# Kernel tuning notes

Hardware: AMD Instinct MI355X
Metric: run time of the kernel (lower is better)

Reference implementation:

```python
import jax, jax.numpy as jnp
import numpy as np

N = 100000
E = 1600000
IN, HID, OUT = 2, 32, 1

def setup_inputs() -> dict:
    key = jax.random.key(0)
    ks = jax.random.split(key, 12)
    x = jax.random.normal(ks[0], (N, IN), dtype=jnp.float32)
    edge_index = jax.random.randint(ks[1], (2, E), 0, N, dtype=jnp.int64)
    def lin(k, i, o):
        s = 1.0 / np.sqrt(i)
        return jax.random.uniform(k, (i, o), jnp.float32, -s, s)
    return {
        "x": x,
        "edge_index": edge_index,
        "w1": lin(ks[2], IN, HID), "b1": jnp.zeros((HID,), jnp.float32),
        "g1": jnp.ones((HID,), jnp.float32), "be1": jnp.zeros((HID,), jnp.float32),
        "w2": lin(ks[3], HID, HID), "b2": jnp.zeros((HID,), jnp.float32),
        "g2": jnp.ones((HID,), jnp.float32), "be2": jnp.zeros((HID,), jnp.float32),
        "w3": lin(ks[4], HID, OUT), "b3": jnp.zeros((OUT,), jnp.float32),
    }

def _gcn_conv(x, src, dst, norm, W, b):
    # x: [N, Fin] -> [N, Fout]; symmetric-normalized aggregation incl. self-loops
    h = x @ W                                  # [N, Fout]
    msg = h[src] * norm[:, None]               # gather + scale, [E+N, Fout]
    out = jax.ops.segment_sum(msg, dst, num_segments=N)  # scatter-add
    return out + b

def _layer_norm(x, g, b, eps=1e-5):
    mu = jnp.mean(x, axis=-1, keepdims=True)
    var = jnp.mean(jnp.square(x - mu), axis=-1, keepdims=True)
    return (x - mu) * jax.lax.rsqrt(var + eps) * g + b

def reference(x, edge_index, w1, b1, g1, be1, w2, b2, g2, be2, w3, b3):
    loops = jnp.arange(N, dtype=edge_index.dtype)
    src = jnp.concatenate([edge_index[0], loops])  # [E+N]
    dst = jnp.concatenate([edge_index[1], loops])
    deg = jax.ops.segment_sum(jnp.ones_like(src, dtype=x.dtype), dst, num_segments=N)
    dinv = jnp.where(deg > 0, jax.lax.rsqrt(deg), 0.0)
    norm = dinv[src] * dinv[dst]                   # [E+N]

    h = _gcn_conv(x, src, dst, norm, w1, b1)
    h = jax.nn.relu(_layer_norm(h, g1, be1))       # dropout = identity (eval)
    h = _gcn_conv(h, src, dst, norm, w2, b2)
    h = jax.nn.relu(_layer_norm(h, g2, be2))
    return _gcn_conv(h, src, dst, norm, w3, b3)
```

## Files before the change

kernel.cpp:

```cpp
#include <hip/hip_runtime.h>
#include <hip/hip_fp16.h>

constexpr int NN  = 100000;
constexpr int NE  = 1600000;
constexpr int NE4 = NE / 4;
constexpr int HID = 32;
constexpr int NPB = 128;
constexpr int NBIN = (NN + NPB - 1) / NPB;
constexpr int NB  = (NN + 255) / 256;

constexpr int NPART = 8;
constexpr int PPB   = (NBIN + NPART - 1) / NPART;
constexpr int NCHUNK = 120;
constexpr int CAP   = 16;
constexpr int QS    = CAP + 1;


__global__ __launch_bounds__(256) void k_binhist(const int* __restrict__ ei,
                                                 int* __restrict__ bincnt) {
  __shared__ int lh[NBIN];
  int t = threadIdx.x;
  for (int b = t; b < NBIN; b += 256) lh[b] = 0;
  __syncthreads();
  const int4* d4 = (const int4*)(ei + NE);
  for (int q = blockIdx.x * 256 + t; q < NE4; q += gridDim.x * 256) {
    int4 v = d4[q];
    atomicAdd(&lh[v.x >> 7], 1);
    atomicAdd(&lh[v.y >> 7], 1);
    atomicAdd(&lh[v.z >> 7], 1);
    atomicAdd(&lh[v.w >> 7], 1);
  }
  __syncthreads();
  for (int b = t; b < NBIN; b += 256) {
    int v = lh[b];
    if (v) atomicAdd(&bincnt[b], v);
  }
}

__global__ __launch_bounds__(1024) void k_binscan(const int* __restrict__ bincnt,
                                                  int* __restrict__ binptr,
                                                  int* __restrict__ cursor) {
  __shared__ int s[1024];
  int t = threadIdx.x;
  int v = (t < NBIN) ? bincnt[t] : 0;
  s[t] = v;
  __syncthreads();
#pragma unroll
  for (int off = 1; off < 1024; off <<= 1) {
    int add = (t >= off) ? s[t - off] : 0;
    __syncthreads();
    s[t] += add;
    __syncthreads();
  }
  if (t < NBIN) {
    int ex = s[t] - v;
    binptr[t] = ex;
    cursor[t] = ex;
  }
  if (t == NBIN - 1) binptr[NBIN] = s[t];
}

__global__ __launch_bounds__(256) void k_wcscatter(const int* __restrict__ ei,
                                                   int* __restrict__ cursor,
                                                   int* __restrict__ be) {
  __shared__ int q[PPB * QS];
  __shared__ int qn[PPB];
  int t = threadIdx.x;
  int part  = blockIdx.x & (NPART - 1);
  int chunk = blockIdx.x >> 3;
  int b0  = part * PPB;
  int bHi = min(b0 + PPB, NBIN);
  int nb  = bHi - b0;
  for (int b = t; b < nb; b += 256) qn[b] = 0;
  int q0 = (int)((long long)NE4 * chunk / NCHUNK);
  int q1 = (int)((long long)NE4 * (chunk + 1) / NCHUNK);
  const int4* d4 = (const int4*)(ei + NE);
  const int4* s4 = (const int4*)ei;
  __syncthreads();
  for (int qbase = q0; qbase < q1; qbase += 256) {
    int qi = qbase + t;
    int4 dv = make_int4(-1, -1, -1, -1);
    int4 sv = make_int4(0, 0, 0, 0);
    if (qi < q1) { dv = d4[qi]; sv = s4[qi]; }
    int val0 = 0, val1 = 0, val2 = 0, val3 = 0;
    int lb0 = 0, lb1 = 0, lb2 = 0, lb3 = 0;
    unsigned pend = 0;
    {
      int bkt = dv.x >> 7;
      if (dv.x >= 0 && bkt >= b0 && bkt < bHi) {
        val0 = sv.x | ((dv.x & (NPB - 1)) << 17);
        lb0 = bkt - b0;
        int slot = atomicAdd(&qn[lb0], 1);
        if (slot < CAP) q[lb0 * QS + slot] = val0; else pend |= 1u;
      }
    }
    {
      int bkt = dv.y >> 7;
      if (dv.y >= 0 && bkt >= b0 && bkt < bHi) {
        val1 = sv.y | ((dv.y & (NPB - 1)) << 17);
        lb1 = bkt - b0;
        int slot = atomicAdd(&qn[lb1], 1);
        if (slot < CAP) q[lb1 * QS + slot] = val1; else pend |= 2u;
      }
    }
    {
      int bkt = dv.z >> 7;
      if (dv.z >= 0 && bkt >= b0 && bkt < bHi) {
        val2 = sv.z | ((dv.z & (NPB - 1)) << 17);
        lb2 = bkt - b0;
        int slot = atomicAdd(&qn[lb2], 1);
        if (slot < CAP) q[lb2 * QS + slot] = val2; else pend |= 4u;
      }
    }
    {
      int bkt = dv.w >> 7;
      if (dv.w >= 0 && bkt >= b0 && bkt < bHi) {
        val3 = sv.w | ((dv.w & (NPB - 1)) << 17);
        lb3 = bkt - b0;
        int slot = atomicAdd(&qn[lb3], 1);
        if (slot < CAP) q[lb3 * QS + slot] = val3; else pend |= 8u;
      }
    }
    for (;;) {
      __syncthreads();
      for (int b = t; b < nb; b += 256) {
        int n = qn[b];
        if (n >= CAP) {
          int pos = atomicAdd(&cursor[b0 + b], CAP);
#pragma unroll
          for (int j = 0; j < CAP; j++) be[pos + j] = q[b * QS + j];
          qn[b] = 0;
        }
      }
      if (!__syncthreads_or(pend ? 1 : 0)) break;
      if (pend & 1u) {
        int slot = atomicAdd(&qn[lb0], 1);
        if (slot < CAP) { q[lb0 * QS + slot] = val0; pend &= ~1u; }
      }
      if (pend & 2u) {
        int slot = atomicAdd(&qn[lb1], 1);
        if (slot < CAP) { q[lb1 * QS + slot] = val1; pend &= ~2u; }
      }
      if (pend & 4u) {
        int slot = atomicAdd(&qn[lb2], 1);
        if (slot < CAP) { q[lb2 * QS + slot] = val2; pend &= ~4u; }
      }
      if (pend & 8u) {
        int slot = atomicAdd(&qn[lb3], 1);
        if (slot < CAP) { q[lb3 * QS + slot] = val3; pend &= ~8u; }
      }
    }
  }
  for (int b = t; b < nb; b += 256) {
    int n = qn[b];
    if (n > 0) {
      int pos = atomicAdd(&cursor[b0 + b], n);
      for (int j = 0; j < n; j++) be[pos + j] = q[b * QS + j];
    }
  }
}

__global__ __launch_bounds__(256) void k_sort(const int* __restrict__ binptr,
                                              const int* __restrict__ be,
                                              const float* __restrict__ x,
                                              int* __restrict__ csr,
                                              int* __restrict__ rowptr,
                                              int* __restrict__ deg,
                                              float* __restrict__ dinv,
                                              float* __restrict__ xs) {
  __shared__ int hist[NPB];
  __shared__ int excl[NPB];
  __shared__ int cur[NPB];
  int t = threadIdx.x, b = blockIdx.x;
  int e0 = binptr[b], e1 = binptr[b + 1];
  if (t < NPB) hist[t] = 0;
  __syncthreads();
  for (int k = e0 + t; k < e1; k += 256) atomicAdd(&hist[be[k] >> 17], 1);
  __syncthreads();
  if (t < NPB) excl[t] = hist[t];
  __syncthreads();
#pragma unroll
  for (int off = 1; off < NPB; off <<= 1) {
    int add = 0;
    if (t < NPB && t >= off) add = excl[t - off];
    __syncthreads();
    if (t < NPB) excl[t] += add;
    __syncthreads();
  }
  if (t < NPB) {
    int ex = excl[t] - hist[t];
    cur[t] = ex;
    int i = b * NPB + t;
    if (i < NN) {
      int dg = hist[t];
      deg[i] = dg;
      rowptr[i] = e0 + ex;
      float d = rsqrtf((float)dg + 1.0f);
      dinv[i] = d;
      float2 xv = ((const float2*)x)[i];
      ((float2*)xs)[i] = make_float2(d * xv.x, d * xv.y);
    }
  }
  __syncthreads();
  for (int k = e0 + t; k < e1; k += 256) {
    int v = be[k];
    int pos = atomicAdd(&cur[v >> 17], 1);
    csr[e0 + pos] = v & 0x1FFFF;
  }
}


__global__ __launch_bounds__(256) void k_l1(const int* __restrict__ rowptr,
                                            const int* __restrict__ deg,
                                            const int* __restrict__ csr,
                                            const float* __restrict__ dinv,
                                            const float* __restrict__ xs,
                                            const float* __restrict__ w1,
                                            const float* __restrict__ b1,
                                            const float* __restrict__ g1,
                                            const float* __restrict__ be1,
                                            __half* __restrict__ h1s) {
  __shared__ float w1s[64], b1s[32], g1s[32], be1s[32];
  int t = threadIdx.x;
  if (t < 64) w1s[t] = w1[t];
  if (t < 32) { b1s[t] = b1[t]; g1s[t] = g1[t]; be1s[t] = be1[t]; }
  __syncthreads();
  int i = blockIdx.x * 256 + t;
  if (i >= NN) return;
  const float2* xs2 = (const float2*)xs;
  float2 sv = xs2[i];
  float in0 = sv.x, in1 = sv.y;
  int r0 = rowptr[i], dg = deg[i];
  int k = 0;
  for (; k + 4 <= dg; k += 4) {
    int s0 = csr[r0 + k], s1 = csr[r0 + k + 1];
    int s2 = csr[r0 + k + 2], s3 = csr[r0 + k + 3];
    float2 v0 = xs2[s0], v1 = xs2[s1], v2 = xs2[s2], v3 = xs2[s3];
    in0 += v0.x; in1 += v0.y;
    in0 += v1.x; in1 += v1.y;
    in0 += v2.x; in1 += v2.y;
    in0 += v3.x; in1 += v3.y;
  }
  for (; k < dg; k++) {
    int s = csr[r0 + k];
    float2 v = xs2[s];
    in0 += v.x; in1 += v.y;
  }
  float di = dinv[i];
  float a0 = di * in0, a1 = di * in1;
  float h[HID];
  float mu = 0.f;
#pragma unroll
  for (int j = 0; j < HID; j++) {
    h[j] = fmaf(a0, w1s[j], fmaf(a1, w1s[32 + j], b1s[j]));
    mu += h[j];
  }
  mu *= (1.0f / HID);
  float var = 0.f;
#pragma unroll
  for (int j = 0; j < HID; j++) { float dd = h[j] - mu; var += dd * dd; }
  var *= (1.0f / HID);
  float rstd = rsqrtf(var + 1e-5f);
  __half2* o2 = (__half2*)(h1s + (size_t)i * HID);
#pragma unroll
  for (int q = 0; q < 8; q++) {
    float vx = di * fmaxf(fmaf((h[4 * q]     - mu) * rstd, g1s[4 * q],     be1s[4 * q]),     0.f);
    float vy = di * fmaxf(fmaf((h[4 * q + 1] - mu) * rstd, g1s[4 * q + 1], be1s[4 * q + 1]), 0.f);
    float vz = di * fmaxf(fmaf((h[4 * q + 2] - mu) * rstd, g1s[4 * q + 2], be1s[4 * q + 2]), 0.f);
    float vw = di * fmaxf(fmaf((h[4 * q + 3] - mu) * rstd, g1s[4 * q + 3], be1s[4 * q + 3]), 0.f);
    o2[2 * q]     = __floats2half2_rn(vx, vy);
    o2[2 * q + 1] = __floats2half2_rn(vz, vw);
  }
}

__global__ __launch_bounds__(256) void k_l2(const int* __restrict__ rowptr,
                                            const int* __restrict__ deg,
                                            const int* __restrict__ csr,
                                            const float* __restrict__ dinv,
                                            const __half* __restrict__ h1s,
                                            const float* __restrict__ w2,
                                            const float* __restrict__ b2,
                                            const float* __restrict__ g2,
                                            const float* __restrict__ be2,
                                            const float* __restrict__ w3,
                                            float* __restrict__ ps) {
  __shared__ float w2s[HID * HID];
  __shared__ float b2s[32], g2s[32], be2s[32], w3s[32];
  __shared__ float aggl[8][HID];
  int t = threadIdx.x;
  for (int u = t; u < HID * HID; u += 256) w2s[u] = w2[u];
  if (t < 32) { b2s[t] = b2[t]; g2s[t] = g2[t]; be2s[t] = be2[t]; w3s[t] = w3[t]; }
  __syncthreads();
  int g = t >> 5;
  int L = t & 31;
  int i = blockIdx.x * 8 + g;
  int jg = L >> 3, c4 = L & 7;
  float ax = 0.f, ay = 0.f, az = 0.f, aw = 0.f;
  auto gather = [&](int s) {
    float2 raw = *(const float2*)(h1s + (size_t)s * HID + c4 * 4);
    __half2 p0 = *(__half2*)&raw.x;
    __half2 p1 = *(__half2*)&raw.y;
    float2 f0 = __half22float2(p0);
    float2 f1 = __half22float2(p1);
    ax += f0.x; ay += f0.y; az += f1.x; aw += f1.y;
  };
  if (jg == 0) gather(i);
  int r0 = rowptr[i], dg = deg[i];
  for (int base = 0; base < dg; base += 16) {
#pragma unroll
    for (int it = 0; it < 4; it++) {
      int kk = base + it * 4 + jg;
      int sv = csr[r0 + kk];
      int s = (kk < dg) ? sv : NN;
      gather(s);
    }
  }
  ax += __shfl_xor(ax, 8, 32);  ay += __shfl_xor(ay, 8, 32);
  az += __shfl_xor(az, 8, 32);  aw += __shfl_xor(aw, 8, 32);
  ax += __shfl_xor(ax, 16, 32); ay += __shfl_xor(ay, 16, 32);
  az += __shfl_xor(az, 16, 32); aw += __shfl_xor(aw, 16, 32);
  float di = dinv[i];
  if (jg == 0) {
    aggl[g][c4 * 4 + 0] = di * ax;
    aggl[g][c4 * 4 + 1] = di * ay;
    aggl[g][c4 * 4 + 2] = di * az;
    aggl[g][c4 * 4 + 3] = di * aw;
  }
  __syncthreads();
  float h = b2s[L];
#pragma unroll
  for (int k = 0; k < HID; k++) h = fmaf(aggl[g][k], w2s[k * HID + L], h);
  float mu = h;
#pragma unroll
  for (int off = 16; off > 0; off >>= 1) mu += __shfl_xor(mu, off, 32);
  mu *= (1.0f / HID);
  float dd = h - mu;
  float var = dd * dd;
#pragma unroll
  for (int off = 16; off > 0; off >>= 1) var += __shfl_xor(var, off, 32);
  var *= (1.0f / HID);
  float rstd = rsqrtf(var + 1e-5f);
  float v = fmaf(dd * rstd, g2s[L], be2s[L]);
  v = fmaxf(v, 0.0f);
  float pi = v * w3s[L];
#pragma unroll
  for (int off = 16; off > 0; off >>= 1) pi += __shfl_xor(pi, off, 32);
  if (L == 0) ps[i] = di * pi;
}

__global__ __launch_bounds__(256) void k_l3(const int* __restrict__ rowptr,
                                            const int* __restrict__ deg,
                                            const int* __restrict__ csr,
                                            const float* __restrict__ dinv,
                                            const float* __restrict__ ps,
                                            const float* __restrict__ b3,
                                            float* __restrict__ out) {
  int i = blockIdx.x * 256 + threadIdx.x;
  if (i >= NN) return;
  float inner = ps[i];
  int r0 = rowptr[i], dg = deg[i];
  int k = 0;
  for (; k + 4 <= dg; k += 4) {
    float v0 = ps[csr[r0 + k]],     v1 = ps[csr[r0 + k + 1]];
    float v2 = ps[csr[r0 + k + 2]], v3 = ps[csr[r0 + k + 3]];
    inner += v0; inner += v1; inner += v2; inner += v3;
  }
  for (; k < dg; k++) inner += ps[csr[r0 + k]];
  out[i] = fmaf(dinv[i], inner, b3[0]);
}


extern "C" void kernel_launch(void* const* d_in, const int* in_sizes, int n_in,
                              void* d_out, int out_size, void* d_ws, size_t ws_size,
                              hipStream_t stream) {
  const float* x   = (const float*)d_in[0];
  const int*   ei  = (const int*)d_in[1];
  const float* w1  = (const float*)d_in[2];
  const float* b1  = (const float*)d_in[3];
  const float* g1  = (const float*)d_in[4];
  const float* be1 = (const float*)d_in[5];
  const float* w2  = (const float*)d_in[6];
  const float* b2  = (const float*)d_in[7];
  const float* g2  = (const float*)d_in[8];
  const float* be2 = (const float*)d_in[9];
  const float* w3  = (const float*)d_in[10];
  const float* b3  = (const float*)d_in[11];
  float* out = (float*)d_out;

  char* wp = (char*)d_ws;
  auto alloc = [&](size_t bytes) {
    char* r = wp;
    wp += (bytes + 255) & ~size_t(255);
    return r;
  };
  int*    bincnt = (int*)alloc((size_t)NBIN * 4);
  int*    binptr = (int*)alloc((size_t)(NBIN + 1) * 4);
  int*    cursor = (int*)alloc((size_t)NBIN * 4);
  int*    bedge  = (int*)alloc((size_t)NE * 4);
  int*    csr    = (int*)alloc((size_t)(NE + 32) * 4);
  int*    rowptr = (int*)alloc((size_t)NN * 4);
  int*    deg    = (int*)alloc((size_t)NN * 4);
  float*  dinv   = (float*)alloc((size_t)NN * 4);
  float*  xs     = (float*)alloc((size_t)NN * 2 * 4);
  __half* h1s    = (__half*)alloc((size_t)(NN + 1) * HID * 2);
  float*  ps     = (float*)alloc((size_t)NN * 4);

  hipMemsetAsync(bincnt, 0, (size_t)NBIN * 4, stream);
  hipMemsetAsync(h1s + (size_t)NN * HID, 0, HID * 2, stream);
  k_binhist  <<<NB, 256, 0, stream>>>(ei, bincnt);
  k_binscan  <<<1, 1024, 0, stream>>>(bincnt, binptr, cursor);
  k_wcscatter<<<NCHUNK * NPART, 256, 0, stream>>>(ei, cursor, bedge);
  k_sort     <<<NBIN, 256, 0, stream>>>(binptr, bedge, x, csr, rowptr, deg, dinv, xs);
  k_l1       <<<NB, 256, 0, stream>>>(rowptr, deg, csr, dinv, xs, w1, b1, g1, be1, h1s);
  k_l2       <<<NN / 8, 256, 0, stream>>>(rowptr, deg, csr, dinv, h1s,
                                          w2, b2, g2, be2, w3, ps);
  k_l3       <<<NB, 256, 0, stream>>>(rowptr, deg, csr, dinv, ps, b3, out);
}
```

Before: 221.0 us.

## Pad CSR rows to 16, vectorize layer-2 gather, skip unneeded source loads

Each CSR row is padded to a multiple of 16 entries, placed at a bin-strided base and filled with a dummy index. This lets the layer-2 kernel read neighbor indices as int4 and gather 8 halves per lane via float4 loads. Layer 2 also drops its shared-memory aggregate and block barrier, broadcasting aggregates with shuffles and computing layer-norm variance in one pass from sum and sum of squares. The scatter kernel only loads source indices when a lane has an in-partition edge, and its chunk count is doubled. The cost is a larger CSR buffer, extra padding writes, and a one-pass variance that can lose some precision.

```diff
diff --git a/kernel.cpp b/kernel.cpp
--- a/kernel.cpp
+++ b/kernel.cpp
@@ -11,9 +11,10 @@
 
 constexpr int NPART = 8;
 constexpr int PPB   = (NBIN + NPART - 1) / NPART;
-constexpr int NCHUNK = 120;
+constexpr int NCHUNK = 240;
 constexpr int CAP   = 16;
 constexpr int QS    = CAP + 1;
+constexpr int BSTRIDE = 2048;
 
 
 __global__ __launch_bounds__(256) void k_binhist(const int* __restrict__ ei,
@@ -80,46 +81,39 @@
   for (int qbase = q0; qbase < q1; qbase += 256) {
     int qi = qbase + t;
     int4 dv = make_int4(-1, -1, -1, -1);
+    if (qi < q1) dv = d4[qi];
+    bool in0 = dv.x >= 0 && (dv.x >> 7) >= b0 && (dv.x >> 7) < bHi;
+    bool in1 = dv.y >= 0 && (dv.y >> 7) >= b0 && (dv.y >> 7) < bHi;
+    bool in2 = dv.z >= 0 && (dv.z >> 7) >= b0 && (dv.z >> 7) < bHi;
+    bool in3 = dv.w >= 0 && (dv.w >> 7) >= b0 && (dv.w >> 7) < bHi;
     int4 sv = make_int4(0, 0, 0, 0);
-    if (qi < q1) { dv = d4[qi]; sv = s4[qi]; }
+    if (in0 || in1 || in2 || in3) sv = s4[qi];
     int val0 = 0, val1 = 0, val2 = 0, val3 = 0;
     int lb0 = 0, lb1 = 0, lb2 = 0, lb3 = 0;
     unsigned pend = 0;
-    {
-      int bkt = dv.x >> 7;
-      if (dv.x >= 0 && bkt >= b0 && bkt < bHi) {
-        val0 = sv.x | ((dv.x & (NPB - 1)) << 17);
-        lb0 = bkt - b0;
-        int slot = atomicAdd(&qn[lb0], 1);
-        if (slot < CAP) q[lb0 * QS + slot] = val0; else pend |= 1u;
-      }
-    }
-    {
-      int bkt = dv.y >> 7;
-      if (dv.y >= 0 && bkt >= b0 && bkt < bHi) {
-        val1 = sv.y | ((dv.y & (NPB - 1)) << 17);
-        lb1 = bkt - b0;
-        int slot = atomicAdd(&qn[lb1], 1);
-        if (slot < CAP) q[lb1 * QS + slot] = val1; else pend |= 2u;
-      }
-    }
-    {
-      int bkt = dv.z >> 7;
-      if (dv.z >= 0 && bkt >= b0 && bkt < bHi) {
-        val2 = sv.z | ((dv.z & (NPB - 1)) << 17);
-        lb2 = bkt - b0;
-        int slot = atomicAdd(&qn[lb2], 1);
-        if (slot < CAP) q[lb2 * QS + slot] = val2; else pend |= 4u;
-      }
-    }
-    {
-      int bkt = dv.w >> 7;
-      if (dv.w >= 0 && bkt >= b0 && bkt < bHi) {
-        val3 = sv.w | ((dv.w & (NPB - 1)) << 17);
-        lb3 = bkt - b0;
-        int slot = atomicAdd(&qn[lb3], 1);
-        if (slot < CAP) q[lb3 * QS + slot] = val3; else pend |= 8u;
-      }
+    if (in0) {
+      val0 = sv.x | ((dv.x & (NPB - 1)) << 17);
+      lb0 = (dv.x >> 7) - b0;
+      int slot = atomicAdd(&qn[lb0], 1);
+      if (slot < CAP) q[lb0 * QS + slot] = val0; else pend |= 1u;
+    }
+    if (in1) {
+      val1 = sv.y | ((dv.y & (NPB - 1)) << 17);
+      lb1 = (dv.y >> 7) - b0;
+      int slot = atomicAdd(&qn[lb1], 1);
+      if (slot < CAP) q[lb1 * QS + slot] = val1; else pend |= 2u;
+    }
+    if (in2) {
+      val2 = sv.z | ((dv.z & (NPB - 1)) << 17);
+      lb2 = (dv.z >> 7) - b0;
+      int slot = atomicAdd(&qn[lb2], 1);
+      if (slot < CAP) q[lb2 * QS + slot] = val2; else pend |= 4u;
+    }
+    if (in3) {
+      val3 = sv.w | ((dv.w & (NPB - 1)) << 17);
+      lb3 = (dv.w >> 7) - b0;
+      int slot = atomicAdd(&qn[lb3], 1);
+      if (slot < CAP) q[lb3 * QS + slot] = val3; else pend |= 8u;
     }
     for (;;) {
       __syncthreads();
@@ -171,13 +165,15 @@
   __shared__ int hist[NPB];
   __shared__ int excl[NPB];
   __shared__ int cur[NPB];
+  __shared__ int sbase;
   int t = threadIdx.x, b = blockIdx.x;
   int e0 = binptr[b], e1 = binptr[b + 1];
   if (t < NPB) hist[t] = 0;
+  if (t == 0) sbase = ((binptr[b] + BSTRIDE * b) + 15) & ~15;
   __syncthreads();
   for (int k = e0 + t; k < e1; k += 256) atomicAdd(&hist[be[k] >> 17], 1);
   __syncthreads();
-  if (t < NPB) excl[t] = hist[t];
+  if (t < NPB) excl[t] = (hist[t] + 15) & ~15;
   __syncthreads();
 #pragma unroll
   for (int off = 1; off < NPB; off <<= 1) {
@@ -187,25 +183,28 @@
     if (t < NPB) excl[t] += add;
     __syncthreads();
   }
+  int base = sbase;
   if (t < NPB) {
-    int ex = excl[t] - hist[t];
+    int psz = (hist[t] + 15) & ~15;
+    int ex = excl[t] - psz;
     cur[t] = ex;
     int i = b * NPB + t;
     if (i < NN) {
       int dg = hist[t];
       deg[i] = dg;
-      rowptr[i] = e0 + ex;
+      rowptr[i] = base + ex;
       float d = rsqrtf((float)dg + 1.0f);
       dinv[i] = d;
       float2 xv = ((const float2*)x)[i];
       ((float2*)xs)[i] = make_float2(d * xv.x, d * xv.y);
+      for (int k2 = ex + dg; k2 < ex + psz; k2++) csr[base + k2] = NN;
     }
   }
   __syncthreads();
   for (int k = e0 + t; k < e1; k += 256) {
     int v = be[k];
     int pos = atomicAdd(&cur[v >> 17], 1);
-    csr[e0 + pos] = v & 0x1FFFF;
+    csr[base + pos] = v & 0x1FFFF;
   }
 }
 
@@ -286,7 +285,6 @@
                                             float* __restrict__ ps) {
   __shared__ float w2s[HID * HID];
   __shared__ float b2s[32], g2s[32], be2s[32], w3s[32];
-  __shared__ float aggl[8][HID];
   int t = threadIdx.x;
   for (int u = t; u < HID * HID; u += 256) w2s[u] = w2[u];
   if (t < 32) { b2s[t] = b2[t]; g2s[t] = g2[t]; be2s[t] = be2[t]; w3s[t] = w3[t]; }
@@ -294,53 +292,72 @@
   int g = t >> 5;
   int L = t & 31;
   int i = blockIdx.x * 8 + g;
-  int jg = L >> 3, c4 = L & 7;
-  float ax = 0.f, ay = 0.f, az = 0.f, aw = 0.f;
+  int jg = L >> 2, c4 = L & 3;
+  float a0 = 0.f, a1 = 0.f, a2 = 0.f, a3 = 0.f;
+  float a4 = 0.f, a5 = 0.f, a6 = 0.f, a7 = 0.f;
   auto gather = [&](int s) {
-    float2 raw = *(const float2*)(h1s + (size_t)s * HID + c4 * 4);
+    float4 raw = *(const float4*)(h1s + (size_t)s * HID + c4 * 8);
     __half2 p0 = *(__half2*)&raw.x;
     __half2 p1 = *(__half2*)&raw.y;
+    __half2 p2 = *(__half2*)&raw.z;
+    __half2 p3 = *(__half2*)&raw.w;
     float2 f0 = __half22float2(p0);
     float2 f1 = __half22float2(p1);
-    ax += f0.x; ay += f0.y; az += f1.x; aw += f1.y;
+    float2 f2 = __half22float2(p2);
+    float2 f3 = __half22float2(p3);
+    a0 += f0.x; a1 += f0.y; a2 += f1.x; a3 += f1.y;
+    a4 += f2.x; a5 += f2.y; a6 += f3.x; a7 += f3.y;
   };
   if (jg == 0) gather(i);
-  int r0 = rowptr[i], dg = deg[i];
-  for (int base = 0; base < dg; base += 16) {
-#pragma unroll
-    for (int it = 0; it < 4; it++) {
-      int kk = base + it * 4 + jg;
-      int sv = csr[r0 + kk];
-      int s = (kk < dg) ? sv : NN;
-      gather(s);
-    }
-  }
-  ax += __shfl_xor(ax, 8, 32);  ay += __shfl_xor(ay, 8, 32);
-  az += __shfl_xor(az, 8, 32);  aw += __shfl_xor(aw, 8, 32);
-  ax += __shfl_xor(ax, 16, 32); ay += __shfl_xor(ay, 16, 32);
-  az += __shfl_xor(az, 16, 32); aw += __shfl_xor(aw, 16, 32);
+  int r0 = rowptr[i];
+  int dgp = (deg[i] + 15) & ~15;
+  const int4* csr4 = (const int4*)(csr + r0);
+  for (int base = 0; base < dgp; base += 32) {
+    int rem = dgp - base;
+    int4 iv = (jg * 4 < rem) ? csr4[(base >> 2) + jg]
+                             : make_int4(NN, NN, NN, NN);
+    gather(iv.x);
+    gather(iv.y);
+    gather(iv.z);
+    gather(iv.w);
+  }
+#pragma unroll
+  for (int off = 4; off <= 16; off <<= 1) {
+    a0 += __shfl_xor(a0, off, 32); a1 += __shfl_xor(a1, off, 32);
+    a2 += __shfl_xor(a2, off, 32); a3 += __shfl_xor(a3, off, 32);
+    a4 += __shfl_xor(a4, off, 32); a5 += __shfl_xor(a5, off, 32);
+    a6 += __shfl_xor(a6, off, 32); a7 += __shfl_xor(a7, off, 32);
+  }
   float di = dinv[i];
-  if (jg == 0) {
-    aggl[g][c4 * 4 + 0] = di * ax;
-    aggl[g][c4 * 4 + 1] = di * ay;
-    aggl[g][c4 * 4 + 2] = di * az;
-    aggl[g][c4 * 4 + 3] = di * aw;
-  }
-  __syncthreads();
+  a0 *= di; a1 *= di; a2 *= di; a3 *= di;
+  a4 *= di; a5 *= di; a6 *= di; a7 *= di;
   float h = b2s[L];
 #pragma unroll
-  for (int k = 0; k < HID; k++) h = fmaf(aggl[g][k], w2s[k * HID + L], h);
-  float mu = h;
-#pragma unroll
-  for (int off = 16; off > 0; off >>= 1) mu += __shfl_xor(mu, off, 32);
-  mu *= (1.0f / HID);
-  float dd = h - mu;
-  float var = dd * dd;
-#pragma unroll
-  for (int off = 16; off > 0; off >>= 1) var += __shfl_xor(var, off, 32);
-  var *= (1.0f / HID);
+  for (int k = 0; k < HID; k++) {
+    float src;
+    switch (k & 7) {
+      case 0: src = a0; break;
+      case 1: src = a1; break;
+      case 2: src = a2; break;
+      case 3: src = a3; break;
+      case 4: src = a4; break;
+      case 5: src = a5; break;
+      case 6: src = a6; break;
+      default: src = a7; break;
+    }
+    float ak = __shfl(src, k >> 3, 32);
+    h = fmaf(ak, w2s[k * HID + L], h);
+  }
+  float s1 = h, s2 = h * h;
+#pragma unroll
+  for (int off = 16; off > 0; off >>= 1) {
+    s1 += __shfl_xor(s1, off, 32);
+    s2 += __shfl_xor(s2, off, 32);
+  }
+  float mu = s1 * (1.0f / HID);
+  float var = fmaxf(s2 * (1.0f / HID) - mu * mu, 0.0f);
   float rstd = rsqrtf(var + 1e-5f);
-  float v = fmaf(dd * rstd, g2s[L], be2s[L]);
+  float v = fmaf((h - mu) * rstd, g2s[L], be2s[L]);
   v = fmaxf(v, 0.0f);
   float pi = v * w3s[L];
 #pragma unroll
@@ -397,7 +414,7 @@
   int*    binptr = (int*)alloc((size_t)(NBIN + 1) * 4);
   int*    cursor = (int*)alloc((size_t)NBIN * 4);
   int*    bedge  = (int*)alloc((size_t)NE * 4);
-  int*    csr    = (int*)alloc((size_t)(NE + 32) * 4);
+  int*    csr    = (int*)alloc((size_t)(NE + (size_t)NBIN * BSTRIDE + 64) * 4);
   int*    rowptr = (int*)alloc((size_t)NN * 4);
   int*    deg    = (int*)alloc((size_t)NN * 4);
   float*  dinv   = (float*)alloc((size_t)NN * 4);
```

After: 219.4 us. No clear change (-0.7%).
